# Kernel tuning notes

Measured on AMD Instinct MI355X. Metric: run time of the kernel, lower is better.

Reference implementation:

```python
import jax, jax.numpy as jnp
import numpy as np

B, S, D, V = 8, 128, 1024, 32000
TEMP, TOP_K, TOP_P = 1.0, 50, 0.95
NEG_INF = jnp.float32(-jnp.inf)


def setup_inputs() -> dict:
    key = jax.random.key(0)
    k1, k2, k3, k4 = jax.random.split(key, 4)
    return {
        "psi_real": jax.random.normal(k1, (B, S, D), dtype=jnp.float32),
        "psi_imag": jax.random.normal(k2, (B, S, D), dtype=jnp.float32),
        "W_r": jax.random.normal(k3, (V, D), dtype=jnp.float32) * (1.0 / np.sqrt(D)),
        "W_i": jax.random.normal(k4, (V, D), dtype=jnp.float32) * (1.0 / np.sqrt(D)),
        "bias": jnp.zeros((V,), dtype=jnp.float32),
    }


def reference(psi_real, psi_imag, W_r, W_i, bias):
    # Complex projection: (psi_r + i psi_i) @ (W_r + i W_i)^T
    amp_r = jnp.einsum("bsd,vd->bsv", psi_real, W_r) - jnp.einsum("bsd,vd->bsv", psi_imag, W_i)
    amp_i = jnp.einsum("bsd,vd->bsv", psi_imag, W_r) + jnp.einsum("bsd,vd->bsv", psi_real, W_i)
    amp_sq = amp_r * amp_r + amp_i * amp_i  # Born rule |amp|^2, [B,S,V]
    floor = jnp.mean(amp_sq, axis=-1, keepdims=True) * 1e-6 + 1e-30
    logits = (jnp.log(amp_sq + floor) + bias) / max(TEMP, 1e-8)
    log_probs = jax.nn.log_softmax(logits, axis=-1)

    # top-k filter: keep values >= k-th largest
    kth = jax.lax.top_k(logits, TOP_K)[0][..., -1:]
    filt = jnp.where(logits < kth, NEG_INF, logits)

    # top-p (nucleus) filter on the top-k-filtered logits
    order = jnp.argsort(-filt, axis=-1)                      # descending sort indices
    sorted_logits = jnp.take_along_axis(filt, order, axis=-1)
    sp = jax.nn.softmax(sorted_logits, axis=-1)
    cum = jnp.cumsum(sp, axis=-1)
    drop = (cum - sp) >= TOP_P                               # cumulative prob excluding current token
    sorted_filt = jnp.where(drop, NEG_INF, sorted_logits)
    inv = jnp.argsort(order, axis=-1)                        # scatter back to original order
    filt2 = jnp.take_along_axis(sorted_filt, inv, axis=-1)

    probs = jax.nn.softmax(filt2, axis=-1)
    tokens = jax.random.categorical(jax.random.key(42), filt2, axis=-1)  # multinomial sample [B,S]
    return logits, log_probs, amp_sq, tokens, probs
```

## Files before the change

### kernel.cpp

```cpp
#include <hip/hip_runtime.h>

#define BS   1024
#define DD   1024
#define VV   32000
#define TOPK 50
#define TOPPF 0.95f
#define NVTOT 32768000ull

typedef __attribute__((ext_vector_type(8))) short bf16x8;
typedef __attribute__((ext_vector_type(4))) float f32x4;
typedef __attribute__((ext_vector_type(4))) int   i32x4;

#define MFMA(A,B,C) __builtin_amdgcn_mfma_f32_16x16x32_bf16(A, B, C, 0, 0, 0)

__device__ __forceinline__ unsigned fkey(float f) {
  unsigned u = __float_as_uint(f);
  return (u & 0x80000000u) ? ~u : (u | 0x80000000u);
}
__device__ __forceinline__ unsigned rotl32(unsigned x, int r) {
  return (x << r) | (x >> (32 - r));
}
__device__ __forceinline__ ushort f2bf(float f) {
  unsigned u = __float_as_uint(f);
  unsigned r = ((u >> 16) & 1u) + 0x7FFFu;
  return (ushort)((u + r) >> 16);
}
__device__ __forceinline__ float bf2f(ushort h) {
  return __uint_as_float(((unsigned)h) << 16);
}
__device__ __forceinline__ bf16x8 negbf(bf16x8 a) {
  i32x4 t = __builtin_bit_cast(i32x4, a);
  t = t ^ 0x80008000;
  return __builtin_bit_cast(bf16x8, t);
}

__device__ float gumbel_at(unsigned i) {
  unsigned x0 = 0u, x1 = i;
  const unsigned ks0 = 0u, ks1 = 42u, ks2 = 0x1BD11BDAu ^ 0u ^ 42u;
  x0 += ks0; x1 += ks1;
  const int rotA[4] = {13, 15, 26, 6};
  const int rotB[4] = {17, 29, 16, 24};
#define TF_R4(R) { x0 += x1; x1 = rotl32(x1, R[0]); x1 ^= x0; \
                   x0 += x1; x1 = rotl32(x1, R[1]); x1 ^= x0; \
                   x0 += x1; x1 = rotl32(x1, R[2]); x1 ^= x0; \
                   x0 += x1; x1 = rotl32(x1, R[3]); x1 ^= x0; }
  TF_R4(rotA); x0 += ks1; x1 += ks2 + 1u;
  TF_R4(rotB); x0 += ks2; x1 += ks0 + 2u;
  TF_R4(rotA); x0 += ks0; x1 += ks1 + 3u;
  TF_R4(rotB); x0 += ks1; x1 += ks2 + 4u;
  TF_R4(rotA); x0 += ks2; x1 += ks0 + 5u;
#undef TF_R4
  unsigned bits = x0 ^ x1;
  float f = __uint_as_float(0x3F800000u | (bits >> 9)) - 1.0f;
  float u = fmaxf(f, 1.17549435e-38f);
  return -logf(-logf(u));
}

__global__ __launch_bounds__(256) void pack_split(
    const float* __restrict__ xr, const float* __restrict__ xi,
    ushort* __restrict__ ohr, ushort* __restrict__ olr,
    ushort* __restrict__ ohi, ushort* __restrict__ oli,
    float si, int n4) {
  int g = blockIdx.x * 256 + threadIdx.x;
  if (g >= n4) return;
  int i = g * 4;
  float4 a = *(const float4*)(xr + i);
  float4 b = *(const float4*)(xi + i);
  float av[4] = {a.x, a.y, a.z, a.w};
  float bv[4] = {b.x * si, b.y * si, b.z * si, b.w * si};
  unsigned hr[4], lr[4], hi_[4], li[4];
#pragma unroll
  for (int j = 0; j < 4; ++j) {
    ushort h = f2bf(av[j]);          hr[j] = h;
    lr[j] = f2bf(av[j] - bf2f(h));
    ushort h2 = f2bf(bv[j]);         hi_[j] = h2;
    li[j] = f2bf(bv[j] - bf2f(h2));
  }
  uint2 w;
  w.x = hr[0] | (hr[1] << 16); w.y = hr[2] | (hr[3] << 16);
  *(uint2*)(ohr + i) = w;
  w.x = lr[0] | (lr[1] << 16); w.y = lr[2] | (lr[3] << 16);
  *(uint2*)(olr + i) = w;
  w.x = hi_[0] | (hi_[1] << 16); w.y = hi_[2] | (hi_[3] << 16);
  *(uint2*)(ohi + i) = w;
  w.x = li[0] | (li[1] << 16); w.y = li[2] | (li[3] << 16);
  *(uint2*)(oli + i) = w;
}

__global__ __launch_bounds__(512) void gemm_mfma(
    const ushort* __restrict__ APk,
    const ushort* __restrict__ Wrh, const ushort* __restrict__ Wrl,
    const ushort* __restrict__ Wih, const ushort* __restrict__ Wil,
    float* __restrict__ amp) {
  __shared__ ushort lds[2][8][4096];
  const int tid = threadIdx.x;
  const int lane = tid & 63, wid = tid >> 6;
  const int d = blockIdx.x;
  const int x = d & 7, s = d >> 3;
  const int bm = ((x >> 1) << 1) | (s & 1);
  const int bn = (x & 1) * 125 + (s >> 1);
  const int row0 = bm << 7, col0 = bn << 7;
  const int wm = wid >> 2, wn = wid & 3;

  const ushort* tp[8] = {APk, APk + (1 << 20), APk + (2 << 20), APk + (3 << 20),
                         Wrh, Wrl, Wih, Wil};

  const int rrow = tid >> 2;
  const int ss = (tid & 3) ^ (rrow & 3) ^ ((rrow >> 2) & 3);
  const size_t offA = (size_t)(row0 + rrow) * DD + (ss << 3);
  const size_t offB = (size_t)(col0 + rrow) * DD + (ss << 3);

  f32x4 accr[4][2] = {}, acci[4][2] = {};

  int aoff[4], boff[2];
#pragma unroll
  for (int m = 0; m < 4; ++m) {
    const int ar = (wm << 6) + (m << 4) + (lane & 15);
    aoff[m] = (ar << 6) + ((((lane >> 4)) ^ (ar & 3) ^ ((ar >> 2) & 3)) << 4);
  }
#pragma unroll
  for (int n = 0; n < 2; ++n) {
    const int br = (wn << 5) + (n << 4) + (lane & 15);
    boff[n] = (br << 6) + ((((lane >> 4)) ^ (br & 3) ^ ((br >> 2) & 3)) << 4);
  }

#define STAGE(buf, step) {                                                   \
    const int k0 = (step) << 5;                                              \
    _Pragma("unroll")                                                        \
    for (int t = 0; t < 8; ++t) {                                            \
      const ushort* src = tp[t] + ((t < 4) ? offA : offB) + k0;              \
      __builtin_amdgcn_global_load_lds(                                      \
          (const __attribute__((address_space(1))) unsigned int*)src,        \
          (__attribute__((address_space(3))) unsigned int*)&lds[buf][t][wid << 9], \
          16, 0, 0);                                                         \
    }                                                                        \
  }

  STAGE(0, 0);
  __syncthreads();
  int cur = 0;
  for (int step = 0; step < 32; ++step) {
    if (step + 1 < 32) STAGE(cur ^ 1, step + 1);
    const char* L0 = (const char*)&lds[cur][0][0];
    const char* L1 = (const char*)&lds[cur][1][0];
    const char* L2 = (const char*)&lds[cur][2][0];
    const char* L3 = (const char*)&lds[cur][3][0];
    const char* L4 = (const char*)&lds[cur][4][0];
    const char* L5 = (const char*)&lds[cur][5][0];
    const char* L6 = (const char*)&lds[cur][6][0];
    const char* L7 = (const char*)&lds[cur][7][0];

    bf16x8 bRh[2], bRl[2], bIh[2], bIl[2];
#pragma unroll
    for (int n = 0; n < 2; ++n) {
      bRh[n] = *(const bf16x8*)(L4 + boff[n]);
      bRl[n] = *(const bf16x8*)(L5 + boff[n]);
      bIh[n] = *(const bf16x8*)(L6 + boff[n]);
      bIl[n] = *(const bf16x8*)(L7 + boff[n]);
    }
#pragma unroll
    for (int m = 0; m < 4; ++m) {
      bf16x8 aPrh = *(const bf16x8*)(L0 + aoff[m]);
      bf16x8 aPrl = *(const bf16x8*)(L1 + aoff[m]);
      bf16x8 aNih = *(const bf16x8*)(L2 + aoff[m]);
      bf16x8 aNil = *(const bf16x8*)(L3 + aoff[m]);
      bf16x8 aPih = negbf(aNih);
      bf16x8 aPil = negbf(aNil);
      __builtin_amdgcn_s_setprio(1);
#pragma unroll
      for (int n = 0; n < 2; ++n) {
        f32x4 r = accr[m][n], q = acci[m][n];
        r = MFMA(aPrh, bRh[n], r); r = MFMA(aPrh, bRl[n], r); r = MFMA(aPrl, bRh[n], r);
        r = MFMA(aNih, bIh[n], r); r = MFMA(aNih, bIl[n], r); r = MFMA(aNil, bIh[n], r);
        q = MFMA(aPih, bRh[n], q); q = MFMA(aPih, bRl[n], q); q = MFMA(aPil, bRh[n], q);
        q = MFMA(aPrh, bIh[n], q); q = MFMA(aPrh, bIl[n], q); q = MFMA(aPrl, bIh[n], q);
        accr[m][n] = r; acci[m][n] = q;
      }
      __builtin_amdgcn_s_setprio(0);
    }
    __syncthreads();
    cur ^= 1;
  }
#undef STAGE
#pragma unroll
  for (int m = 0; m < 4; ++m)
#pragma unroll
    for (int n = 0; n < 2; ++n)
#pragma unroll
      for (int qi = 0; qi < 4; ++qi) {
        const int row = row0 + (wm << 6) + (m << 4) + ((lane >> 4) << 2) + qi;
        const int col = col0 + (wn << 5) + (n << 4) + (lane & 15);
        float vr = accr[m][n][qi], vi = acci[m][n][qi];
        amp[(size_t)row * VV + col] = vr * vr + vi * vi;
      }
}

__global__ __launch_bounds__(512) void post_row(
    const float* __restrict__ amp, const float* __restrict__ bias,
    float* __restrict__ logits, float* __restrict__ logprobs,
    float* __restrict__ probs, float* __restrict__ tokens) {
  __shared__ __align__(16) float lg[VV];
  __shared__ int hist[4096];
  __shared__ int iscan[512];
  __shared__ float red[512];
  __shared__ float sval[768]; __shared__ int sidx[768];
  __shared__ float ssv[768];  __shared__ int ssi[768];
  __shared__ int scnt;
  __shared__ float sh_f[4];
  __shared__ int   sh_i[4];

  const int row = blockIdx.x, tid = threadIdx.x;
  const float* A = amp + (size_t)row * VV;
  float* Lg = logits + (size_t)row * VV;
  float* Lp = logprobs + (size_t)row * VV;
  float* P  = probs + (size_t)row * VV;

  float s = 0.f;
  for (int i = tid; i < VV / 4; i += 512) {
    float4 a = ((const float4*)A)[i];
    ((float4*)lg)[i] = a;
    s += a.x + a.y + a.z + a.w;
  }
  red[tid] = s; __syncthreads();
  for (int o = 256; o > 0; o >>= 1) { if (tid < o) red[tid] += red[tid + o]; __syncthreads(); }
  if (tid == 0) sh_f[0] = red[0] * (1.0f / (float)VV) * 1e-6f + 1e-30f;
  __syncthreads();
  const float floorv = sh_f[0];
  __syncthreads();

  float mx = -INFINITY;
  for (int i = tid; i < VV / 4; i += 512) {
    float4 a = ((float4*)lg)[i];
    float4 b = ((const float4*)bias)[i];
    float4 l;
    l.x = logf(a.x + floorv) + b.x;
    l.y = logf(a.y + floorv) + b.y;
    l.z = logf(a.z + floorv) + b.z;
    l.w = logf(a.w + floorv) + b.w;
    ((float4*)lg)[i] = l;
    ((float4*)Lg)[i] = l;
    mx = fmaxf(mx, fmaxf(fmaxf(l.x, l.y), fmaxf(l.z, l.w)));
  }
  red[tid] = mx; __syncthreads();
  for (int o = 256; o > 0; o >>= 1) { if (tid < o) red[tid] = fmaxf(red[tid], red[tid + o]); __syncthreads(); }
  mx = red[0]; __syncthreads();

  float se = 0.f;
  for (int i = tid; i < VV / 4; i += 512) {
    float4 l = ((float4*)lg)[i];
    se += expf(l.x - mx) + expf(l.y - mx) + expf(l.z - mx) + expf(l.w - mx);
  }
  red[tid] = se; __syncthreads();
  for (int o = 256; o > 0; o >>= 1) { if (tid < o) red[tid] += red[tid + o]; __syncthreads(); }
  const float lse = mx + logf(red[0]);
  __syncthreads();

  for (int i = tid; i < VV / 4; i += 512) {
    float4 l = ((float4*)lg)[i];
    float4 o4 = {l.x - lse, l.y - lse, l.z - lse, l.w - lse};
    ((float4*)Lp)[i] = o4;
  }

  for (int i = tid; i < 4096; i += 512) hist[i] = 0;
  if (tid == 0) scnt = 0;
  __syncthreads();
  for (int v = tid; v < VV; v += 512)
    atomicAdd(&hist[fkey(lg[v]) >> 20], 1);
  __syncthreads();
  {
    const int hi = 4095 - 8 * tid;
    int part = 0;
#pragma unroll
    for (int j = 0; j < 8; ++j) part += hist[hi - j];
    iscan[tid] = part;
    __syncthreads();
    for (int off = 1; off < 512; off <<= 1) {
      int add = (tid >= off) ? iscan[tid - off] : 0;
      __syncthreads();
      iscan[tid] += add;
      __syncthreads();
    }
    int cum = iscan[tid], prev = tid ? iscan[tid - 1] : 0;
    if (cum >= TOPK && prev < TOPK) sh_i[0] = tid;
    __syncthreads();
    if (tid == 0) {
      int tc = sh_i[0];
      int c = tc ? iscan[tc - 1] : 0;
      int b = 4095 - 8 * tc;
      for (int j = 0; j < 8; ++j) {
        int h = hist[4095 - 8 * tc - j];
        if (c + h >= TOPK) { b = 4095 - 8 * tc - j; break; }
        c += h;
      }
      sh_i[1] = b;
    }
    __syncthreads();
  }
  const unsigned binb = (unsigned)sh_i[1];

  for (int v = tid; v < VV; v += 512) {
    if ((fkey(lg[v]) >> 20) >= binb) {
      int p = atomicAdd(&scnt, 1);
      if (p < 768) { sval[p] = lg[v]; sidx[p] = v; }
    }
  }
  __syncthreads();
  const int n = min(scnt, 768);
  for (int i = tid; i < n; i += 512) {
    float vi = sval[i]; int ii = sidx[i]; int r = 0;
    for (int j = 0; j < n; ++j) {
      float vj = sval[j]; int ij = sidx[j];
      r += (vj > vi) || (vj == vi && ij < ii);
    }
    ssv[r] = vi; ssi[r] = ii;
  }
  __syncthreads();
  if (tid == 0) {
    const float kthv = ssv[TOPK - 1];
    int np = TOPK;
    while (np < n && ssv[np] >= kthv) ++np;
    const float mx2 = ssv[0];
    float denom = 0.f;
    for (int j = 0; j < np; ++j) denom += expf(ssv[j] - mx2);
    float cum = 0.f; int m = np;
    for (int j = 0; j < np; ++j) {
      float sp = expf(ssv[j] - mx2) / denom;
      cum += sp;
      if (cum - sp >= TOPPF) { m = j; break; }
    }
    float dk = 0.f;
    for (int j = 0; j < m; ++j) dk += expf(ssv[j] - mx2);
    sh_f[1] = mx2; sh_f[2] = dk; sh_f[3] = ssv[m - 1];
    sh_i[2] = ssi[m - 1];
  }
  __syncthreads();
  const float mx2 = sh_f[1], dk = sh_f[2], vb = sh_f[3];
  const int ib = sh_i[2];

  float best = -INFINITY; int bidx = 0x7FFFFFFF;
  for (int i = tid; i < VV / 4; i += 512) {
    float4 l4 = ((float4*)lg)[i];
    float lv[4] = {l4.x, l4.y, l4.z, l4.w};
    float4 p4 = {0.f, 0.f, 0.f, 0.f};
    float pv[4] = {0.f, 0.f, 0.f, 0.f};
#pragma unroll
    for (int j = 0; j < 4; ++j) {
      const int v = i * 4 + j;
      float l = lv[j];
      bool kept = (l > vb) || (l == vb && v <= ib);
      if (kept) {
        pv[j] = expf(l - mx2) / dk;
        float g = gumbel_at((unsigned)(row * VV + v));
        float sc = l + g;
        if (sc > best || (sc == best && v < bidx)) { best = sc; bidx = v; }
      }
    }
    p4.x = pv[0]; p4.y = pv[1]; p4.z = pv[2]; p4.w = pv[3];
    ((float4*)P)[i] = p4;
  }
  red[tid] = best; iscan[tid] = bidx; __syncthreads();
  for (int o = 256; o > 0; o >>= 1) {
    if (tid < o) {
      if (red[tid + o] > red[tid] ||
          (red[tid + o] == red[tid] && iscan[tid + o] < iscan[tid])) {
        red[tid] = red[tid + o]; iscan[tid] = iscan[tid + o];
      }
    }
    __syncthreads();
  }
  if (tid == 0) tokens[row] = (float)iscan[0];
}

extern "C" void kernel_launch(void* const* d_in, const int* in_sizes, int n_in,
                              void* d_out, int out_size, void* d_ws, size_t ws_size,
                              hipStream_t stream) {
  const float* pr   = (const float*)d_in[0];
  const float* pi   = (const float*)d_in[1];
  const float* wr   = (const float*)d_in[2];
  const float* wi   = (const float*)d_in[3];
  const float* bias = (const float*)d_in[4];

  float* out      = (float*)d_out;
  float* logits   = out;
  float* logprobs = out + NVTOT;
  float* ampsq    = out + 2 * NVTOT;
  float* tokens   = out + 3 * NVTOT;
  float* probs    = out + 3 * NVTOT + 1024;

  ushort* Wrh = (ushort*)logits;
  ushort* Wrl = Wrh + 32768000;
  ushort* Wih = (ushort*)logprobs;
  ushort* Wil = Wih + 32768000;
  ushort* APk = (ushort*)probs;

  pack_split<<<1024, 256, 0, stream>>>(pr, pi,
      APk, APk + (1 << 20), APk + (2 << 20), APk + (3 << 20), -1.0f, 262144);
  pack_split<<<32000, 256, 0, stream>>>(wr, wi,
      Wrh, Wrl, Wih, Wil, 1.0f, 8192000);

  gemm_mfma<<<2000, 512, 0, stream>>>(APk, Wrh, Wrl, Wih, Wil, ampsq);

  post_row<<<BS, 512, 0, stream>>>(ampsq, bias, logits, logprobs, probs, tokens);
}
```

Before: 1.017 ms.

## Switch GEMM to 32x32x16 MFMA with 256x256 block tiles

Moves the split-bf16 complex GEMM from 16x16x32 MFMA on 128x128 tiles to 32x32x16 MFMA on 256x256 tiles with K-step 16. The LDS staging layout, swizzle and block-to-tile mapping are redone to fit, and the grid shrinks from 2000 to 500 blocks. The aim is more operand reuse per loaded byte and fewer instructions per flop. The costs are 500 blocks being fewer than two waves across the CUs, much larger accumulator register use (32 f32x16 vectors per thread) that may cause spills or low occupancy, and twice as many barrier-separated steps. The s_setprio hints are also removed.

```diff
diff --git a/kernel.cpp b/kernel.cpp
--- a/kernel.cpp
+++ b/kernel.cpp
@@ -7,11 +7,12 @@
 #define TOPPF 0.95f
 #define NVTOT 32768000ull
 
-typedef __attribute__((ext_vector_type(8))) short bf16x8;
-typedef __attribute__((ext_vector_type(4))) float f32x4;
-typedef __attribute__((ext_vector_type(4))) int   i32x4;
-
-#define MFMA(A,B,C) __builtin_amdgcn_mfma_f32_16x16x32_bf16(A, B, C, 0, 0, 0)
+typedef __attribute__((ext_vector_type(8)))  short bf16x8;
+typedef __attribute__((ext_vector_type(4)))  float f32x4;
+typedef __attribute__((ext_vector_type(16))) float f32x16;
+typedef __attribute__((ext_vector_type(4)))  int   i32x4;
+
+#define MFMA32(A,B,C) __builtin_amdgcn_mfma_f32_32x32x16_bf16(A, B, C, 0, 0, 0)
 
 __device__ __forceinline__ unsigned fkey(float f) {
   unsigned u = __float_as_uint(f);
@@ -87,7 +88,7 @@
   *(uint2*)(oli + i) = w;
 }
 
-__global__ __launch_bounds__(512) void gemm_mfma(
+__global__ __launch_bounds__(512, 2) void gemm_mfma(
     const ushort* __restrict__ APk,
     const ushort* __restrict__ Wrh, const ushort* __restrict__ Wrl,
     const ushort* __restrict__ Wih, const ushort* __restrict__ Wil,
@@ -95,43 +96,44 @@
   __shared__ ushort lds[2][8][4096];
   const int tid = threadIdx.x;
   const int lane = tid & 63, wid = tid >> 6;
+
   const int d = blockIdx.x;
-  const int x = d & 7, s = d >> 3;
-  const int bm = ((x >> 1) << 1) | (s & 1);
-  const int bn = (x & 1) * 125 + (s >> 1);
-  const int row0 = bm << 7, col0 = bn << 7;
+  const int xx = d & 7, ii = d >> 3;
+  const int seq = (xx < 4 ? xx * 63 : 252 + (xx - 4) * 62) + ii;
+  const int bm = seq & 3, bn = seq >> 2;
+  const int row0 = bm << 8, col0 = bn << 8;
   const int wm = wid >> 2, wn = wid & 3;
 
   const ushort* tp[8] = {APk, APk + (1 << 20), APk + (2 << 20), APk + (3 << 20),
                          Wrh, Wrl, Wih, Wil};
 
-  const int rrow = tid >> 2;
-  const int ss = (tid & 3) ^ (rrow & 3) ^ ((rrow >> 2) & 3);
-  const size_t offA = (size_t)(row0 + rrow) * DD + (ss << 3);
-  const size_t offB = (size_t)(col0 + rrow) * DD + (ss << 3);
-
-  f32x4 accr[4][2] = {}, acci[4][2] = {};
+  const int rr = tid >> 1, hh = tid & 1;
+  const int srck = hh ^ ((rr >> 2) & 1);
+  const size_t offA = (size_t)(row0 + rr) * DD + (srck << 3);
+  const size_t offB = (size_t)(col0 + rr) * DD + (srck << 3);
+
+  f32x16 accr[4][2] = {}, acci[4][2] = {};
 
   int aoff[4], boff[2];
 #pragma unroll
   for (int m = 0; m < 4; ++m) {
-    const int ar = (wm << 6) + (m << 4) + (lane & 15);
-    aoff[m] = (ar << 6) + ((((lane >> 4)) ^ (ar & 3) ^ ((ar >> 2) & 3)) << 4);
+    const int ar = (wm << 7) + (m << 5) + (lane & 31);
+    aoff[m] = (ar << 5) + (((lane >> 5) ^ ((ar >> 2) & 1)) << 4);
   }
 #pragma unroll
   for (int n = 0; n < 2; ++n) {
-    const int br = (wn << 5) + (n << 4) + (lane & 15);
-    boff[n] = (br << 6) + ((((lane >> 4)) ^ (br & 3) ^ ((br >> 2) & 3)) << 4);
+    const int br = (wn << 6) + (n << 5) + (lane & 31);
+    boff[n] = (br << 5) + (((lane >> 5) ^ ((br >> 2) & 1)) << 4);
   }
 
 #define STAGE(buf, step) {                                                   \
-    const int k0 = (step) << 5;                                              \
+    const int k0 = (step) << 4;                                              \
     _Pragma("unroll")                                                        \
     for (int t = 0; t < 8; ++t) {                                            \
       const ushort* src = tp[t] + ((t < 4) ? offA : offB) + k0;              \
       __builtin_amdgcn_global_load_lds(                                      \
           (const __attribute__((address_space(1))) unsigned int*)src,        \
-          (__attribute__((address_space(3))) unsigned int*)&lds[buf][t][wid << 9], \
+          (__attribute__((address_space(3))) unsigned int*)&lds[buf][t][tid << 3], \
           16, 0, 0);                                                         \
     }                                                                        \
   }
@@ -139,8 +141,8 @@
   STAGE(0, 0);
   __syncthreads();
   int cur = 0;
-  for (int step = 0; step < 32; ++step) {
-    if (step + 1 < 32) STAGE(cur ^ 1, step + 1);
+  for (int step = 0; step < 64; ++step) {
+    if (step + 1 < 64) STAGE(cur ^ 1, step + 1);
     const char* L0 = (const char*)&lds[cur][0][0];
     const char* L1 = (const char*)&lds[cur][1][0];
     const char* L2 = (const char*)&lds[cur][2][0];
@@ -166,17 +168,15 @@
       bf16x8 aNil = *(const bf16x8*)(L3 + aoff[m]);
       bf16x8 aPih = negbf(aNih);
       bf16x8 aPil = negbf(aNil);
-      __builtin_amdgcn_s_setprio(1);
 #pragma unroll
       for (int n = 0; n < 2; ++n) {
-        f32x4 r = accr[m][n], q = acci[m][n];
-        r = MFMA(aPrh, bRh[n], r); r = MFMA(aPrh, bRl[n], r); r = MFMA(aPrl, bRh[n], r);
-        r = MFMA(aNih, bIh[n], r); r = MFMA(aNih, bIl[n], r); r = MFMA(aNil, bIh[n], r);
-        q = MFMA(aPih, bRh[n], q); q = MFMA(aPih, bRl[n], q); q = MFMA(aPil, bRh[n], q);
-        q = MFMA(aPrh, bIh[n], q); q = MFMA(aPrh, bIl[n], q); q = MFMA(aPrl, bIh[n], q);
+        f32x16 r = accr[m][n], q = acci[m][n];
+        r = MFMA32(aPrh, bRh[n], r); r = MFMA32(aPrh, bRl[n], r); r = MFMA32(aPrl, bRh[n], r);
+        r = MFMA32(aNih, bIh[n], r); r = MFMA32(aNih, bIl[n], r); r = MFMA32(aNil, bIh[n], r);
+        q = MFMA32(aPih, bRh[n], q); q = MFMA32(aPih, bRl[n], q); q = MFMA32(aPil, bRh[n], q);
+        q = MFMA32(aPrh, bIh[n], q); q = MFMA32(aPrh, bIl[n], q); q = MFMA32(aPrl, bIh[n], q);
         accr[m][n] = r; acci[m][n] = q;
       }
-      __builtin_amdgcn_s_setprio(0);
     }
     __syncthreads();
     cur ^= 1;
@@ -185,14 +185,17 @@
 #pragma unroll
   for (int m = 0; m < 4; ++m)
 #pragma unroll
-    for (int n = 0; n < 2; ++n)
-#pragma unroll
-      for (int qi = 0; qi < 4; ++qi) {
-        const int row = row0 + (wm << 6) + (m << 4) + ((lane >> 4) << 2) + qi;
-        const int col = col0 + (wn << 5) + (n << 4) + (lane & 15);
-        float vr = accr[m][n][qi], vi = acci[m][n][qi];
-        amp[(size_t)row * VV + col] = vr * vr + vi * vi;
+    for (int n = 0; n < 2; ++n) {
+      f32x16 r = accr[m][n], q = acci[m][n];
+      const int colg = col0 + (wn << 6) + (n << 5) + (lane & 31);
+      const int rowb = row0 + (wm << 7) + (m << 5) + ((lane >> 5) << 2);
+#pragma unroll
+      for (int reg = 0; reg < 16; ++reg) {
+        const int row = rowb + (reg & 3) + ((reg >> 2) << 3);
+        float vr = r[reg], vi = q[reg];
+        amp[(size_t)row * VV + colg] = vr * vr + vi * vi;
       }
+    }
 }
 
 __global__ __launch_bounds__(512) void post_row(
@@ -398,7 +401,7 @@
   pack_split<<<32000, 256, 0, stream>>>(wr, wi,
       Wrh, Wrl, Wih, Wil, 1.0f, 8192000);
 
-  gemm_mfma<<<2000, 512, 0, stream>>>(APk, Wrh, Wrl, Wih, Wil, ampsq);
+  gemm_mfma<<<500, 512, 0, stream>>>(APk, Wrh, Wrl, Wih, Wil, ampsq);
 
   post_row<<<BS, 512, 0, stream>>>(ampsq, bias, logits, logprobs, probs, tokens);
 }
```

Measured after the change: 2.433 ms. 2.39x slower.
